# Performance work log

Hardware: AMD Instinct MI355X
Metric: run time of the kernel (lower is better)

## Reference

```python
import jax, jax.numpy as jnp
import numpy as np
import math

DIFF = True   # params['diff'] -> kind='random_walk'
SHIFT = 0.0   # params['shift']
MIN_WINDOW = 10
EPS = 1e-6


def _window_sizes(T):
    ws = []
    cur = math.log10(MIN_WINDOW)
    end = math.log10(T - 1)
    while cur < end:
        w = int(10 ** cur)
        if MIN_WINDOW <= w <= T - 1:
            ws.append(w)
        cur += 0.25
    if T not in ws:
        ws.append(T)
    return sorted(set(ws))


def _hurst_random_walk(x):
    B, T = x.shape
    ws = _window_sizes(T)  # static python list (shapes are static)
    rs_list = []
    for w in ws:
        n = T // w
        seg = x[:, : n * w].reshape(B, n, w)            # (B, n, w)
        d = seg[..., 1:] - seg[..., :-1]                # (B, n, w-1)
        mean_inc = (seg[..., -1] - seg[..., 0]) / (w - 1)
        dev = d - mean_inc[..., None]
        Z = jnp.cumsum(dev, axis=-1)                    # rescaled-range scan
        R = jnp.max(Z, axis=-1) - jnp.min(Z, axis=-1)   # (B, n)
        S = jnp.std(d, axis=-1, ddof=1)                 # unbiased std
        rs_list.append(jnp.mean(R / (S + EPS), axis=-1))
    RS = jnp.stack(rs_list, axis=1)                     # (B, K)
    X = jnp.log10(jnp.asarray(ws, dtype=x.dtype) + EPS) # (K,)
    Y = jnp.log10(RS + EPS)
    Xc = X - jnp.mean(X)
    denom = jnp.sum(Xc * Xc)
    H = jnp.sum((Y - jnp.mean(Y, axis=1, keepdims=True)) * Xc, axis=1) / (denom + EPS)
    H = jnp.where(jnp.isfinite(H), H, jnp.asarray(1.0, x.dtype))
    return H


def setup_inputs() -> dict:
    key = jax.random.key(0)
    x = jax.random.normal(key, (8192, 4096), dtype=jnp.float32)
    return {"x": x}


def reference(x):
    H = _hurst_random_walk(x)
    return (H + SHIFT)[:, None]  # (B, 1)
```

## Files before the change

### kernel.cpp

```cpp
#include <hip/hip_runtime.h>
#include <math.h>
#include <utility>

#define TLEN 4096
#define NW   12
#define BLOCK 256
#define EPSF 1e-6f

typedef float v2f __attribute__((ext_vector_type(2)));

__device__ const float XC_TAB[NW] = {
    -1.3608041f, -1.1303552f, -0.8694424f, -0.6126161f,
    -0.3608041f, -0.1128308f,  0.1388830f,  0.3889322f,
     0.6391959f,  0.8891277f,  1.1391578f,  1.2515558f };
__device__ const float INVN_TAB[NW] = {
    1.0f/409.0f, 1.0f/240.0f, 1.0f/132.0f, 1.0f/73.0f,
    1.0f/40.0f,  1.0f/23.0f,  1.0f/12.0f,  1.0f/7.0f,
    0.25f, 0.5f, 1.0f, 1.0f };
#define INV_DEN 0.11577579f
#define LOG10_2 0.30102999566f

__device__ __forceinline__ float max3f(float a, float b, float c) {
    float r; asm("v_max3_f32 %0, %1, %2, %3" : "=v"(r) : "v"(a), "v"(b), "v"(c)); return r;
}
__device__ __forceinline__ float min3f(float a, float b, float c) {
    float r; asm("v_min3_f32 %0, %1, %2, %3" : "=v"(r) : "v"(a), "v"(b), "v"(c)); return r;
}
__device__ __forceinline__ v2f pk_fma(v2f a, v2f b, v2f c) {
    v2f d; asm("v_pk_fma_f32 %0, %1, %2, %3" : "=v"(d) : "v"(a), "v"(b), "v"(c)); return d;
}
__device__ __forceinline__ v2f pk_add(v2f a, v2f b) {
    v2f d; asm("v_pk_add_f32 %0, %1, %2" : "=v"(d) : "v"(a), "v"(b)); return d;
}

__device__ __forceinline__ float wave_reduce_sum(float v) {
    #pragma unroll
    for (int o = 32; o > 0; o >>= 1) v += __shfl_xor(v, o, 64);
    return v;
}
template<int G>
__device__ __forceinline__ float reduce_leaders(float v) {
    #pragma unroll
    for (int o = G; o < 64; o <<= 1) v += __shfl_xor(v, o, 64);
    return v;
}

template<int FLO, int FHI>
__device__ __forceinline__ float seg_rs2(const float* __restrict__ row,
                                         const float* __restrict__ P4,
                                         int b, int W, float m, float invwm2,
                                         float mx, float mn) {
    float plo = P4[b >> 2];
    if constexpr (FLO > 0) {
        const int k0 = b - FLO;
        #pragma unroll
        for (int t = 0; t < FLO; ++t) {
            float d = row[k0 + t + 1] - row[k0 + t];
            plo = fmaf(d, d, plo);
        }
    }
    const int e = b + W - 1;
    float phi = P4[e >> 2];
    if constexpr (FHI > 0) {
        const int k0 = e - FHI;
        #pragma unroll
        for (int t = 0; t < FHI; ++t) {
            float d = row[k0 + t + 1] - row[k0 + t];
            phi = fmaf(d, d, phi);
        }
    }
    float ss  = phi - plo;
    float var = fmaf(-(float)(W - 1) * m, m, ss) * invwm2;
    float S   = __builtin_amdgcn_sqrtf(fmaxf(var, 0.0f));
    return (mx - mn) * __builtin_amdgcn_rcpf(S + EPSF);
}

template<int LO, int HI, int JB>
__device__ __forceinline__ void chunk_fold(const float4 q, float nm, float& mx, float& mn) {
    if constexpr (LO <= HI) {
        constexpr int NV = HI - LO + 1;
        float v[NV];
        #pragma unroll
        for (int r = 0; r < NV; ++r)
            v[r] = fmaf((float)(JB + LO + r), nm, (&q.x)[LO + r]);
        if constexpr (NV == 1) { mx = fmaxf(mx, v[0]); mn = fminf(mn, v[0]); }
        else if constexpr (NV == 2) { mx = max3f(mx, v[0], v[1]); mn = min3f(mn, v[0], v[1]); }
        else if constexpr (NV == 3) { mx = fmaxf(mx, max3f(v[0], v[1], v[2]));
                                      mn = fminf(mn, min3f(v[0], v[1], v[2])); }
        else { mx = max3f(max3f(mx, v[0], v[1]), v[2], v[3]);
               mn = min3f(min3f(mn, v[0], v[1]), v[2], v[3]); }
    }
}

template<int W, int NSEG, int C>
__device__ __forceinline__ void mchunk_step(const float4* __restrict__ p,
                                            const float (&nm)[NSEG],
                                            float (&mx)[NSEG], float (&mn)[NSEG]) {
    constexpr int E0 = 4 * C;
    constexpr int K0 = E0 / W;
    constexpr int SA = K0 * W;
    constexpr int LOA = (SA == E0) ? 1 : 0;
    constexpr int HIA_ = SA + W - 1 - E0;
    constexpr int HIA = HIA_ < 3 ? HIA_ : 3;
    float4 q = p[C];
    if constexpr (K0 < NSEG)
        chunk_fold<LOA, HIA, E0 - SA>(q, nm[K0], mx[K0], mn[K0]);
    constexpr bool HASB = (K0 + 1 < NSEG) && (SA + W + 1 - E0 <= 3);
    if constexpr (HASB) {
        constexpr int SB = SA + W;
        chunk_fold<SB + 1 - E0, 3, E0 - SB>(q, nm[K0 + 1], mx[K0 + 1], mn[K0 + 1]);
    }
}

template<int W, int NSEG, int... Cs>
__device__ __forceinline__ void mseg_all(const float4* __restrict__ p,
                                         const float (&nm)[NSEG],
                                         float (&mx)[NSEG], float (&mn)[NSEG],
                                         std::integer_sequence<int, Cs...>) {
    (mchunk_step<W, NSEG, Cs>(p, nm, mx, mn), ...);
}

template<int W, int NSEG, int... Ks>
__device__ __forceinline__ float mseg_rs_all(const float* __restrict__ row,
                                             const float* __restrict__ P4, int b,
                                             const float (&m)[NSEG],
                                             const float (&mx)[NSEG], const float (&mn)[NSEG],
                                             std::integer_sequence<int, Ks...>) {
    constexpr float invwm2 = 1.0f / (float)(W - 2);
    float acc = 0.0f;
    ((acc += seg_rs2<(W * Ks) & 3, (W * Ks + W - 1) & 3>(
          row, P4, b + Ks * W, W, m[Ks], invwm2, mx[Ks], mn[Ks])), ...);
    return acc;
}

template<int W, int NSEG>
__device__ __forceinline__ float mseg_task_odd(const float* __restrict__ row,
                                               const float* __restrict__ P4, int b) {
    constexpr int NCH = (W * NSEG + 3) / 4;
    const float4* p = (const float4*)(row + b);
    float nm[NSEG], m[NSEG], mx[NSEG], mn[NSEG];
    #pragma unroll
    for (int k = 0; k < NSEG; ++k) {
        float a0 = row[b + k * W];
        float a1 = row[b + k * W + W - 1];
        m[k] = (a1 - a0) * (1.0f / (float)(W - 1));
        nm[k] = -m[k];
        mx[k] = -INFINITY; mn[k] = INFINITY;
    }
    mseg_all<W, NSEG>(p, nm, mx, mn, std::make_integer_sequence<int, NCH>{});
    return mseg_rs_all<W, NSEG>(row, P4, b, m, mx, mn,
                                std::make_integer_sequence<int, NSEG>{});
}

template<int W, int A, int G>
__device__ __forceinline__ void seg_strided_pk(const float* __restrict__ row, int b, int lane,
                                               float nm, float& mx, float& mn) {
    constexpr int NCH  = (A + W - 1) / 4 + 1;
    constexpr int HIL  = (A + W - 1) & 3;
    constexpr int MAIN_END = (HIL == 3) ? NCH : NCH - 1;
    constexpr int NFULL = MAIN_END - 1;
    constexpr int FULL  = NFULL / G;
    constexpr int REM   = NFULL % G;
    constexpr int NB    = FULL + (REM > 0 ? 1 : 0);
    const float4* p  = (const float4*)(row + (b - A));
    const float4* pl = p + (1 + lane);
    float4 qs[NB > 0 ? NB : 1];
    #pragma unroll
    for (int i = 0; i < FULL; ++i) qs[i] = pl[i * G];
    if constexpr (REM > 0) { if (lane < REM) qs[FULL] = pl[FULL * G]; }
    mx = -INFINITY; mn = INFINITY;
    v2f jc; jc.x = (float)(4 * (1 + lane) - A); jc.y = jc.x + 1.0f;
    const v2f nm2   = {nm, nm};
    const v2f nm2x2 = {nm + nm, nm + nm};
    const v2f step  = {(float)(4 * G), (float)(4 * G)};
    #pragma unroll
    for (int i = 0; i < FULL; ++i) {
        float4 q = qs[i];
        v2f q01 = {q.x, q.y}, q23 = {q.z, q.w};
        v2f t01 = pk_fma(jc, nm2, q01);
        v2f t23 = pk_fma(jc, nm2, pk_add(q23, nm2x2));
        mx = max3f(max3f(mx, t01.x, t01.y), t23.x, t23.y);
        mn = min3f(min3f(mn, t01.x, t01.y), t23.x, t23.y);
        jc = pk_add(jc, step);
    }
    if constexpr (REM > 0) {
        if (lane < REM) {
            float4 q = qs[FULL];
            v2f q01 = {q.x, q.y}, q23 = {q.z, q.w};
            v2f t01 = pk_fma(jc, nm2, q01);
            v2f t23 = pk_fma(jc, nm2, pk_add(q23, nm2x2));
            mx = max3f(max3f(mx, t01.x, t01.y), t23.x, t23.y);
            mn = min3f(min3f(mn, t01.x, t01.y), t23.x, t23.y);
        }
    }
    if constexpr (A < 3) {
        if (lane == 0) chunk_fold<A + 1, 3, -A>(p[0], nm, mx, mn);
    }
    if constexpr (HIL != 3) {
        if (lane == 1) chunk_fold<0, HIL, 4 * (NCH - 1) - A>(p[NCH - 1], nm, mx, mn);
    }
}

template<int W, int A, int G>
__device__ __forceinline__ float group_seg(const float* __restrict__ row,
                                           const float* __restrict__ P4,
                                           int s, int lane) {
    const int b = s * W;
    float a0 = row[b], a1 = row[b + W - 1];
    float m = (a1 - a0) * (1.0f / (float)(W - 1));
    float nm = -m;
    float mx, mn;
    seg_strided_pk<W, A, G>(row, b, lane, nm, mx, mn);
    #pragma unroll
    for (int o = G / 2; o > 0; o >>= 1) {
        mx = fmaxf(mx, __shfl_xor(mx, o, G));
        mn = fminf(mn, __shfl_xor(mn, o, G));
    }
    float r = seg_rs2<A, (A + W - 1) & 3>(
        row, P4, b, W, m, 1.0f / (float)(W - 2), mx, mn);
    return (lane == 0) ? r : 0.0f;
}

__device__ __forceinline__ float w10_seg10(const float (&v)[10], float ss) {
    const float m = (v[9] - v[0]) * (1.0f / 9.0f), nm = -m;
    float x1 = fmaf(1.0f, nm, v[1]);
    float x2 = fmaf(2.0f, nm, v[2]);
    float x3 = fmaf(3.0f, nm, v[3]);
    float x4 = fmaf(4.0f, nm, v[4]);
    float x5 = fmaf(5.0f, nm, v[5]);
    float x6 = fmaf(6.0f, nm, v[6]);
    float x7 = fmaf(7.0f, nm, v[7]);
    float x8 = fmaf(8.0f, nm, v[8]);
    float x9 = fmaf(9.0f, nm, v[9]);
    float mx = max3f(x1, x2, x3);
    mx = max3f(mx, x4, x5); mx = max3f(mx, x6, x7); mx = max3f(mx, x8, x9);
    float mn = min3f(x1, x2, x3);
    mn = min3f(mn, x4, x5); mn = min3f(mn, x6, x7); mn = min3f(mn, x8, x9);
    float var = fmaf(-9.0f * m, m, ss) * 0.125f;
    float S = __builtin_amdgcn_sqrtf(fmaxf(var, 0.0f));
    return (mx - mn) * __builtin_amdgcn_rcpf(S + EPSF);
}

__global__ __launch_bounds__(BLOCK, 7) void hurst_kernel(const float* __restrict__ x,
                                                         float* __restrict__ out) {
    __shared__ __align__(16) float row[TLEN];
    __shared__ __align__(16) float P4[TLEN / 4];
    __shared__ float rs_sum[NW];
    __shared__ float wred[8];

    const int tid = threadIdx.x;
    const int r = blockIdx.x;
    const int w = tid >> 6, l = tid & 63;

    const float4* src = (const float4*)(x + (size_t)r * TLEN);
    float4* dst = (float4*)row;
    #pragma unroll
    for (int i = 0; i < TLEN / 4 / BLOCK; ++i)
        dst[tid + i * BLOCK] = src[tid + i * BLOCK];
    if (tid < NW) rs_sum[tid] = 0.0f;
    __syncthreads();

    {
        float lp1 = 0.0f, lp2 = 0.0f, lp3 = 0.0f, lp4 = 0.0f;
        float total = 0.0f;
        float contrib = 0.0f;
        if (tid < 205) {
            const int b = tid * 20;
            const float4* p = (const float4*)(row + b);
            float4 q0 = p[0], q1 = p[1], q2 = p[2];
            float v[12] = {q0.x,q0.y,q0.z,q0.w, q1.x,q1.y,q1.z,q1.w,
                           q2.x,q2.y,q2.z,q2.w};
            float c = 0.0f, s9 = 0.0f;
            #pragma unroll
            for (int j = 0; j < 10; ++j) {
                if (j == 4) lp1 = c;
                if (j == 8) lp2 = c;
                if (j == 9) s9 = c;
                float d = v[j + 1] - v[j];
                c = fmaf(d, d, c);
            }
            {
                float a1[10] = {v[0],v[1],v[2],v[3],v[4],v[5],v[6],v[7],v[8],v[9]};
                contrib = w10_seg10(a1, s9);
            }
            const float s10 = c;
            const float v10 = v[10], v11 = v[11];
            float d10 = v11 - v10;
            c = fmaf(d10, d10, c);
            if (tid < 204) {
                float4 q3 = p[3], q4 = p[4];
                float u[8] = {q3.x,q3.y,q3.z,q3.w, q4.x,q4.y,q4.z,q4.w};
                float vlast = row[b + 20];
                float d11 = u[0] - v11;
                c = fmaf(d11, d11, c);
                lp3 = c;
                float s19 = 0.0f;
                #pragma unroll
                for (int j = 12; j < 20; ++j) {
                    if (j == 16) lp4 = c;
                    if (j == 19) s19 = c;
                    float nxt = (j + 1 < 20) ? u[j - 11] : vlast;
                    float d = nxt - u[j - 12];
                    c = fmaf(d, d, c);
                }
                float a2[10] = {v10, v11, u[0],u[1],u[2],u[3],u[4],u[5],u[6],u[7]};
                contrib += w10_seg10(a2, s19 - s10);
                total = c;
            } else {
                float4 q3 = p[3];
                float d11 = q3.x - v11;
                c = fmaf(d11, d11, c);
                lp3 = c;
                float d12 = q3.y - q3.x; c = fmaf(d12, d12, c);
                float d13 = q3.z - q3.y; c = fmaf(d13, d13, c);
                float d14 = q3.w - q3.z; c = fmaf(d14, d14, c);
                total = c;
            }
        }
        float incl = total;
        #pragma unroll
        for (int o = 1; o < 64; o <<= 1) {
            float u = __shfl_up(incl, o, 64);
            if (l >= o) incl += u;
        }
        if (l == 63) wred[w] = incl;
        float a = wave_reduce_sum(contrib);
        if (l == 0) atomicAdd(&rs_sum[0], a);
        __syncthreads();
        float off = incl - total;
        #pragma unroll
        for (int w2 = 0; w2 < 4; ++w2)
            if (w2 < w) off += wred[w2];
        if (tid < 204) {
            const int h = tid * 5;
            P4[h]     = off;
            P4[h + 1] = off + lp1;
            P4[h + 2] = off + lp2;
            P4[h + 3] = off + lp3;
            P4[h + 4] = off + lp4;
        } else if (tid == 204) {
            P4[1020] = off;
            P4[1021] = off + lp1;
            P4[1022] = off + lp2;
            P4[1023] = off + lp3;
        }
        __syncthreads();
    }


    {
        float a = group_seg<56, 0, 4>(row, P4, tid >> 2, tid & 3);
        a = reduce_leaders<4>(a);
        if (l == 0) atomicAdd(&rs_sum[3], a);
    }
    {
        float a = group_seg<100, 0, 8>(row, P4, tid >> 3, tid & 7);
        a = reduce_leaders<8>(a);
        if (l == 0) atomicAdd(&rs_sum[4], a);
    }
    {
        const int g4 = (tid >> 4) & 3, gl16 = tid & 15;
        float a = 0.0f;
        if (w == 0) {
            a = group_seg<177, 0, 16>(row, P4, 4 * g4, gl16);
            if (g4 < 2) a += group_seg<177, 0, 16>(row, P4, 4 * (g4 + 4), gl16);
        } else if (w == 1) {
            a = group_seg<177, 1, 16>(row, P4, 4 * g4 + 1, gl16);
            if (g4 < 2) a += group_seg<177, 1, 16>(row, P4, 4 * (g4 + 4) + 1, gl16);
        } else if (w == 2) {
            a = group_seg<177, 2, 16>(row, P4, 4 * g4 + 2, gl16);
            if (g4 < 2) a += group_seg<177, 2, 16>(row, P4, 4 * (g4 + 4) + 2, gl16);
        } else {
            a = group_seg<177, 3, 16>(row, P4, 4 * g4 + 3, gl16);
            if (g4 < 1) a += group_seg<177, 3, 16>(row, P4, 4 * (g4 + 4) + 3, gl16);
        }
        a = reduce_leaders<16>(a);
        if (l == 0) atomicAdd(&rs_sum[5], a);
    }

    if (w == 0) {
        float a = (l < 60) ? mseg_task_odd<17, 4>(row, P4, l * 68) : 0.0f;
        a = wave_reduce_sum(a);
        if (l == 0) atomicAdd(&rs_sum[1], a);
        float c1 = group_seg<316, 0, 16>(row, P4, 8 + ((l >> 4) & 3), l & 15);
        c1 = reduce_leaders<16>(c1);
        if (l == 0) atomicAdd(&rs_sum[6], c1);
    } else if (w == 1) {
        float a = (l < 33) ? mseg_task_odd<31, 4>(row, P4, l * 124) : 0.0f;
        a = wave_reduce_sum(a);
        if (l == 0) atomicAdd(&rs_sum[2], a);
    } else if (w == 2) {
        float c2 = group_seg<100, 0, 8>(row, P4, 32 + (l >> 3), l & 7);
        c2 = reduce_leaders<8>(c2);
        if (l == 0) atomicAdd(&rs_sum[4], c2);
        float c3 = ((l >> 2) < 9) ? group_seg<56, 0, 4>(row, P4, 64 + (l >> 2), l & 3) : 0.0f;
        c3 = reduce_leaders<4>(c3);
        if (l == 0) atomicAdd(&rs_sum[3], c3);
        float c4 = group_seg<562, 2, 32>(row, P4, 1 + 2 * (l >> 5), l & 31);
        c4 = reduce_leaders<32>(c4);
        if (l == 0) atomicAdd(&rs_sum[7], c4);
        float c5 = group_seg<1000, 0, 32>(row, P4, l >> 5, l & 31);
        c5 = reduce_leaders<32>(c5);
        if (l == 0) atomicAdd(&rs_sum[8], c5);
        float c6 = group_seg<316, 0, 16>(row, P4, 4 + ((l >> 4) & 3), l & 15);
        c6 = reduce_leaders<16>(c6);
        if (l == 0) atomicAdd(&rs_sum[6], c6);
    } else {
        float c1 = group_seg<562, 0, 32>(row, P4, 2 * (l >> 5), l & 31);
        c1 += group_seg<562, 0, 32>(row, P4, 4 + 2 * (l >> 5), l & 31);
        float c2 = (l < 32) ? group_seg<562, 2, 32>(row, P4, 5, l & 31) : 0.0f;
        c1 += c2;
        c1 = reduce_leaders<32>(c1);
        if (l == 0) atomicAdd(&rs_sum[7], c1);
        float c3 = group_seg<1000, 0, 32>(row, P4, 2 + (l >> 5), l & 31);
        c3 = reduce_leaders<32>(c3);
        if (l == 0) atomicAdd(&rs_sum[8], c3);
        float c4 = group_seg<316, 0, 16>(row, P4, (l >> 4) & 3, l & 15);
        c4 = reduce_leaders<16>(c4);
        if (l == 0) atomicAdd(&rs_sum[6], c4);
    }


    {
        const int half = tid >> 7, hl = tid & 127;
        const int b = half ? 1778 : 0;
        float m = (row[b + 1777] - row[b]) * (1.0f / 1777.0f);
        float nm = -m, mx, mn;
        if (half == 0) seg_strided_pk<1778, 0, 128>(row, 0,    hl, nm, mx, mn);
        else           seg_strided_pk<1778, 2, 128>(row, 1778, hl, nm, mx, mn);
        #pragma unroll
        for (int o = 32; o > 0; o >>= 1) {
            mx = fmaxf(mx, __shfl_xor(mx, o, 64));
            mn = fminf(mn, __shfl_xor(mn, o, 64));
        }
        if (l == 0) { wred[w * 2] = mx; wred[w * 2 + 1] = mn; }
        __syncthreads();
        if ((tid & 127) == 0) {
            const int wb = tid >> 6;
            float MX = fmaxf(wred[wb * 2],     wred[wb * 2 + 2]);
            float MN = fminf(wred[wb * 2 + 1], wred[wb * 2 + 3]);
            float v;
            if (tid == 0) v = seg_rs2<0, 1>(row, P4, 0,    1778, m, 1.0f / 1776.0f, MX, MN);
            else          v = seg_rs2<2, 3>(row, P4, 1778, 1778, m, 1.0f / 1776.0f, MX, MN);
            atomicAdd(&rs_sum[9], v);
        }
        __syncthreads();
    }
    {
        float m = (row[3161] - row[0]) * (1.0f / 3161.0f);
        float nm = -m, mx, mn;
        seg_strided_pk<3162, 0, 256>(row, 0, tid, nm, mx, mn);
        #pragma unroll
        for (int o = 32; o > 0; o >>= 1) {
            mx = fmaxf(mx, __shfl_xor(mx, o, 64));
            mn = fminf(mn, __shfl_xor(mn, o, 64));
        }
        if (l == 0) { wred[w * 2] = mx; wred[w * 2 + 1] = mn; }
        __syncthreads();
        if (tid == 0) {
            float MX = fmaxf(fmaxf(wred[0], wred[2]), fmaxf(wred[4], wred[6]));
            float MN = fminf(fminf(wred[1], wred[3]), fminf(wred[5], wred[7]));
            atomicAdd(&rs_sum[10],
                      seg_rs2<0, 1>(row, P4, 0, 3162, m, 1.0f / 3160.0f, MX, MN));
        }
        __syncthreads();
    }
    {
        float m = (row[4095] - row[0]) * (1.0f / 4095.0f);
        float nm = -m, mx, mn;
        seg_strided_pk<4096, 0, 256>(row, 0, tid, nm, mx, mn);
        #pragma unroll
        for (int o = 32; o > 0; o >>= 1) {
            mx = fmaxf(mx, __shfl_xor(mx, o, 64));
            mn = fminf(mn, __shfl_xor(mn, o, 64));
        }
        if (l == 0) { wred[w * 2] = mx; wred[w * 2 + 1] = mn; }
        __syncthreads();
        if (tid == 0) {
            float MX = fmaxf(fmaxf(wred[0], wred[2]), fmaxf(wred[4], wred[6]));
            float MN = fminf(fminf(wred[1], wred[3]), fminf(wred[5], wred[7]));
            atomicAdd(&rs_sum[11],
                      seg_rs2<0, 3>(row, P4, 0, 4096, m, 1.0f / 4094.0f, MX, MN));
        }
        __syncthreads();
    }

    if (tid < 64) {
        float t = 0.0f;
        if (tid < NW) {
            float rs = fmaf(rs_sum[tid], INVN_TAB[tid], EPSF);
            t = __builtin_amdgcn_logf(rs) * (LOG10_2) * XC_TAB[tid];
        }
        t = wave_reduce_sum(t);
        if (tid == 0) {
            float h = t * INV_DEN;
            if (!isfinite(h)) h = 1.0f;
            out[r] = h;
        }
    }
}

extern "C" void kernel_launch(void* const* d_in, const int* in_sizes, int n_in,
                              void* d_out, int out_size, void* d_ws, size_t ws_size,
                              hipStream_t stream) {
    const float* x = (const float*)d_in[0];
    float* out = (float*)d_out;
    const int B = out_size;
    hipLaunchKernelGGL(hurst_kernel, dim3(B), dim3(BLOCK), 0, stream, x, out);
}
```

Baseline: 86.22 us.

## Rebalance per-wave segment work and merge large-window reductions into one barrier phase

Splits the W=31 odd-segment task between two waves: one wave handles two segments per task through mseg_task_odd, and a new hand-unrolled helper handles the other two. The 56, 562 and 1000 window groups are redistributed so the four waves carry more even loads. The three large-window passes (1778, 3162, 4096) are fused into one phase with a single shuffle reduction, one barrier, and final R/S computed in parallel by four different threads. The aim is fewer block barriers and less load imbalance between waves, at the cost of more live registers, which could reduce occupancy.

```diff
diff --git a/kernel.cpp b/kernel.cpp
--- a/kernel.cpp
+++ b/kernel.cpp
@@ -150,6 +150,43 @@
     mseg_all<W, NSEG>(p, nm, mx, mn, std::make_integer_sequence<int, NCH>{});
     return mseg_rs_all<W, NSEG>(row, P4, b, m, mx, mn,
                                 std::make_integer_sequence<int, NSEG>{});
+}
+
+__device__ __forceinline__ float w31_odd2(const float* __restrict__ row,
+                                          const float* __restrict__ P4, int mtask) {
+    const int b = 124 * mtask + 62;
+    const float4* p = (const float4*)(row + b - 2);
+    float4 q0 = p[0],  q1 = p[1],  q2 = p[2],  q3 = p[3];
+    float4 q4 = p[4],  q5 = p[5],  q6 = p[6],  q7 = p[7];
+    float4 q8 = p[8],  q9 = p[9],  q10 = p[10], q11 = p[11];
+    float4 q12 = p[12], q13 = p[13], q14 = p[14], q15 = p[15];
+
+    const float m0 = (q8.x - q0.z) * (1.0f / 30.0f), nm0 = -m0;
+    float mx0 = -INFINITY, mn0 = INFINITY;
+    chunk_fold<3, 3, -2>(q0, nm0, mx0, mn0);
+    chunk_fold<0, 3,  2>(q1, nm0, mx0, mn0);
+    chunk_fold<0, 3,  6>(q2, nm0, mx0, mn0);
+    chunk_fold<0, 3, 10>(q3, nm0, mx0, mn0);
+    chunk_fold<0, 3, 14>(q4, nm0, mx0, mn0);
+    chunk_fold<0, 3, 18>(q5, nm0, mx0, mn0);
+    chunk_fold<0, 3, 22>(q6, nm0, mx0, mn0);
+    chunk_fold<0, 3, 26>(q7, nm0, mx0, mn0);
+    chunk_fold<0, 0, 30>(q8, nm0, mx0, mn0);
+
+    const float m1 = (q15.w - q8.y) * (1.0f / 30.0f), nm1 = -m1;
+    float mx1 = -INFINITY, mn1 = INFINITY;
+    chunk_fold<2, 3, -1>(q8,  nm1, mx1, mn1);
+    chunk_fold<0, 3,  3>(q9,  nm1, mx1, mn1);
+    chunk_fold<0, 3,  7>(q10, nm1, mx1, mn1);
+    chunk_fold<0, 3, 11>(q11, nm1, mx1, mn1);
+    chunk_fold<0, 3, 15>(q12, nm1, mx1, mn1);
+    chunk_fold<0, 3, 19>(q13, nm1, mx1, mn1);
+    chunk_fold<0, 3, 23>(q14, nm1, mx1, mn1);
+    chunk_fold<0, 3, 27>(q15, nm1, mx1, mn1);
+
+    float acc = seg_rs2<2, 0>(row, P4, b,      31, m0, 1.0f / 29.0f, mx0, mn0);
+    acc      += seg_rs2<1, 3>(row, P4, b + 31, 31, m1, 1.0f / 29.0f, mx1, mn1);
+    return acc;
 }
 
 template<int W, int A, int G>
@@ -247,6 +284,7 @@
     __shared__ __align__(16) float P4[TLEN / 4];
     __shared__ float rs_sum[NW];
     __shared__ float wred[8];
+    __shared__ float wredB[24];
 
     const int tid = threadIdx.x;
     const int r = blockIdx.x;
@@ -385,34 +423,35 @@
         float c1 = group_seg<316, 0, 16>(row, P4, 8 + ((l >> 4) & 3), l & 15);
         c1 = reduce_leaders<16>(c1);
         if (l == 0) atomicAdd(&rs_sum[6], c1);
+        float c2 = ((l >> 2) < 9) ? group_seg<56, 0, 4>(row, P4, 64 + (l >> 2), l & 3) : 0.0f;
+        c2 = reduce_leaders<4>(c2);
+        if (l == 0) atomicAdd(&rs_sum[3], c2);
     } else if (w == 1) {
-        float a = (l < 33) ? mseg_task_odd<31, 4>(row, P4, l * 124) : 0.0f;
+        float a = (l < 33) ? mseg_task_odd<31, 2>(row, P4, l * 124) : 0.0f;
         a = wave_reduce_sum(a);
         if (l == 0) atomicAdd(&rs_sum[2], a);
+        float c1 = group_seg<562, 0, 32>(row, P4, 2 * (l >> 5), l & 31);
+        c1 += group_seg<562, 0, 32>(row, P4, 4 + 2 * (l >> 5), l & 31);
+        c1 = reduce_leaders<32>(c1);
+        if (l == 0) atomicAdd(&rs_sum[7], c1);
     } else if (w == 2) {
+        float a = (l < 33) ? w31_odd2(row, P4, l) : 0.0f;
+        a = wave_reduce_sum(a);
+        if (l == 0) atomicAdd(&rs_sum[2], a);
+        float c1 = group_seg<316, 0, 16>(row, P4, 4 + ((l >> 4) & 3), l & 15);
+        c1 = reduce_leaders<16>(c1);
+        if (l == 0) atomicAdd(&rs_sum[6], c1);
         float c2 = group_seg<100, 0, 8>(row, P4, 32 + (l >> 3), l & 7);
         c2 = reduce_leaders<8>(c2);
         if (l == 0) atomicAdd(&rs_sum[4], c2);
-        float c3 = ((l >> 2) < 9) ? group_seg<56, 0, 4>(row, P4, 64 + (l >> 2), l & 3) : 0.0f;
-        c3 = reduce_leaders<4>(c3);
-        if (l == 0) atomicAdd(&rs_sum[3], c3);
-        float c4 = group_seg<562, 2, 32>(row, P4, 1 + 2 * (l >> 5), l & 31);
-        c4 = reduce_leaders<32>(c4);
-        if (l == 0) atomicAdd(&rs_sum[7], c4);
-        float c5 = group_seg<1000, 0, 32>(row, P4, l >> 5, l & 31);
-        c5 = reduce_leaders<32>(c5);
-        if (l == 0) atomicAdd(&rs_sum[8], c5);
-        float c6 = group_seg<316, 0, 16>(row, P4, 4 + ((l >> 4) & 3), l & 15);
-        c6 = reduce_leaders<16>(c6);
-        if (l == 0) atomicAdd(&rs_sum[6], c6);
     } else {
-        float c1 = group_seg<562, 0, 32>(row, P4, 2 * (l >> 5), l & 31);
-        c1 += group_seg<562, 0, 32>(row, P4, 4 + 2 * (l >> 5), l & 31);
+        float c1 = group_seg<562, 2, 32>(row, P4, 1 + 2 * (l >> 5), l & 31);
         float c2 = (l < 32) ? group_seg<562, 2, 32>(row, P4, 5, l & 31) : 0.0f;
         c1 += c2;
         c1 = reduce_leaders<32>(c1);
         if (l == 0) atomicAdd(&rs_sum[7], c1);
-        float c3 = group_seg<1000, 0, 32>(row, P4, 2 + (l >> 5), l & 31);
+        float c3 = group_seg<1000, 0, 32>(row, P4, l >> 5, l & 31);
+        c3 += group_seg<1000, 0, 32>(row, P4, 2 + (l >> 5), l & 31);
         c3 = reduce_leaders<32>(c3);
         if (l == 0) atomicAdd(&rs_sum[8], c3);
         float c4 = group_seg<316, 0, 16>(row, P4, (l >> 4) & 3, l & 15);
@@ -420,67 +459,58 @@
         if (l == 0) atomicAdd(&rs_sum[6], c4);
     }
 
-
     {
         const int half = tid >> 7, hl = tid & 127;
-        const int b = half ? 1778 : 0;
-        float m = (row[b + 1777] - row[b]) * (1.0f / 1777.0f);
-        float nm = -m, mx, mn;
-        if (half == 0) seg_strided_pk<1778, 0, 128>(row, 0,    hl, nm, mx, mn);
-        else           seg_strided_pk<1778, 2, 128>(row, 1778, hl, nm, mx, mn);
+        const int b17 = half ? 1778 : 0;
+        float m17 = (row[b17 + 1777] - row[b17]) * (1.0f / 1777.0f);
+        float mx17, mn17;
+        if (half == 0) seg_strided_pk<1778, 0, 128>(row, 0,    hl, -m17, mx17, mn17);
+        else           seg_strided_pk<1778, 2, 128>(row, 1778, hl, -m17, mx17, mn17);
+
+        float m31 = (row[3161] - row[0]) * (1.0f / 3161.0f);
+        float mx31, mn31;
+        seg_strided_pk<3162, 0, 256>(row, 0, tid, -m31, mx31, mn31);
+
+        float m40 = (row[4095] - row[0]) * (1.0f / 4095.0f);
+        float mx40, mn40;
+        seg_strided_pk<4096, 0, 256>(row, 0, tid, -m40, mx40, mn40);
+
         #pragma unroll
         for (int o = 32; o > 0; o >>= 1) {
-            mx = fmaxf(mx, __shfl_xor(mx, o, 64));
-            mn = fminf(mn, __shfl_xor(mn, o, 64));
-        }
-        if (l == 0) { wred[w * 2] = mx; wred[w * 2 + 1] = mn; }
-        __syncthreads();
-        if ((tid & 127) == 0) {
-            const int wb = tid >> 6;
-            float MX = fmaxf(wred[wb * 2],     wred[wb * 2 + 2]);
-            float MN = fminf(wred[wb * 2 + 1], wred[wb * 2 + 3]);
-            float v;
-            if (tid == 0) v = seg_rs2<0, 1>(row, P4, 0,    1778, m, 1.0f / 1776.0f, MX, MN);
-            else          v = seg_rs2<2, 3>(row, P4, 1778, 1778, m, 1.0f / 1776.0f, MX, MN);
-            atomicAdd(&rs_sum[9], v);
-        }
-        __syncthreads();
-    }
-    {
-        float m = (row[3161] - row[0]) * (1.0f / 3161.0f);
-        float nm = -m, mx, mn;
-        seg_strided_pk<3162, 0, 256>(row, 0, tid, nm, mx, mn);
-        #pragma unroll
-        for (int o = 32; o > 0; o >>= 1) {
-            mx = fmaxf(mx, __shfl_xor(mx, o, 64));
-            mn = fminf(mn, __shfl_xor(mn, o, 64));
-        }
-        if (l == 0) { wred[w * 2] = mx; wred[w * 2 + 1] = mn; }
+            mx17 = fmaxf(mx17, __shfl_xor(mx17, o, 64));
+            mn17 = fminf(mn17, __shfl_xor(mn17, o, 64));
+            mx31 = fmaxf(mx31, __shfl_xor(mx31, o, 64));
+            mn31 = fminf(mn31, __shfl_xor(mn31, o, 64));
+            mx40 = fmaxf(mx40, __shfl_xor(mx40, o, 64));
+            mn40 = fminf(mn40, __shfl_xor(mn40, o, 64));
+        }
+        if (l == 0) {
+            float* wb = wredB + w * 6;
+            wb[0] = mx17; wb[1] = mn17;
+            wb[2] = mx31; wb[3] = mn31;
+            wb[4] = mx40; wb[5] = mn40;
+        }
         __syncthreads();
         if (tid == 0) {
-            float MX = fmaxf(fmaxf(wred[0], wred[2]), fmaxf(wred[4], wred[6]));
-            float MN = fminf(fminf(wred[1], wred[3]), fminf(wred[5], wred[7]));
+            float MX = fmaxf(wredB[0], wredB[6]);
+            float MN = fminf(wredB[1], wredB[7]);
+            atomicAdd(&rs_sum[9],
+                      seg_rs2<0, 1>(row, P4, 0, 1778, m17, 1.0f / 1776.0f, MX, MN));
+        } else if (tid == 128) {
+            float MX = fmaxf(wredB[12], wredB[18]);
+            float MN = fminf(wredB[13], wredB[19]);
+            atomicAdd(&rs_sum[9],
+                      seg_rs2<2, 3>(row, P4, 1778, 1778, m17, 1.0f / 1776.0f, MX, MN));
+        } else if (tid == 64) {
+            float MX = fmaxf(fmaxf(wredB[2], wredB[8]),  fmaxf(wredB[14], wredB[20]));
+            float MN = fminf(fminf(wredB[3], wredB[9]),  fminf(wredB[15], wredB[21]));
             atomicAdd(&rs_sum[10],
-                      seg_rs2<0, 1>(row, P4, 0, 3162, m, 1.0f / 3160.0f, MX, MN));
-        }
-        __syncthreads();
-    }
-    {
-        float m = (row[4095] - row[0]) * (1.0f / 4095.0f);
-        float nm = -m, mx, mn;
-        seg_strided_pk<4096, 0, 256>(row, 0, tid, nm, mx, mn);
-        #pragma unroll
-        for (int o = 32; o > 0; o >>= 1) {
-            mx = fmaxf(mx, __shfl_xor(mx, o, 64));
-            mn = fminf(mn, __shfl_xor(mn, o, 64));
-        }
-        if (l == 0) { wred[w * 2] = mx; wred[w * 2 + 1] = mn; }
-        __syncthreads();
-        if (tid == 0) {
-            float MX = fmaxf(fmaxf(wred[0], wred[2]), fmaxf(wred[4], wred[6]));
-            float MN = fminf(fminf(wred[1], wred[3]), fminf(wred[5], wred[7]));
+                      seg_rs2<0, 1>(row, P4, 0, 3162, m31, 1.0f / 3160.0f, MX, MN));
+        } else if (tid == 192) {
+            float MX = fmaxf(fmaxf(wredB[4], wredB[10]), fmaxf(wredB[16], wredB[22]));
+            float MN = fminf(fminf(wredB[5], wredB[11]), fminf(wredB[17], wredB[23]));
             atomicAdd(&rs_sum[11],
-                      seg_rs2<0, 3>(row, P4, 0, 4096, m, 1.0f / 4094.0f, MX, MN));
+                      seg_rs2<0, 3>(row, P4, 0, 4096, m40, 1.0f / 4094.0f, MX, MN));
         }
         __syncthreads();
     }
```

New measurement: 87.47 us. Within noise of the previous version (+1.4%).
